# Kernel optimization log

Measured on AMD Instinct MI355X. Metric: run time of the kernel, lower is better.

Reference implementation:

```python
import jax, jax.numpy as jnp
import numpy as np

NEG_INF = -1e9  # large negative instead of -inf for safe masked softmax
LRELU_ALPHA = 0.2


def setup_inputs() -> dict:
    key = jax.random.key(0)
    k1, k2, k3, k4, k5 = jax.random.split(key, 5)
    B, N, Din, H, F = 8, 1024, 256, 4, 64
    X = jax.random.normal(k1, (B, N, Din), dtype=jnp.float32)
    A = jax.random.randint(k2, (B, N, N), 0, 2).astype(jnp.int32)
    # xavier-ish scaled params
    W = jax.random.normal(k3, (Din, H * F), dtype=jnp.float32) * np.sqrt(2.0 / (Din + H * F))
    a_src = jax.random.normal(k4, (H, F), dtype=jnp.float32) * np.sqrt(2.0 / (1 + F))
    a_dst = jax.random.normal(k5, (H, F), dtype=jnp.float32) * np.sqrt(2.0 / (1 + F))
    return {"X": X, "A": A, "W": W, "a_src": a_src, "a_dst": a_dst}


def reference(X, A, W, a_src, a_dst):
    B, N, _ = X.shape
    H, F = a_src.shape
    Wh = (X @ W).reshape(B, N, H, F)                       # [B,N,H,F]
    e_src = jnp.einsum('bnhf,hf->bnh', Wh, a_src)          # [B,N,H]
    e_dst = jnp.einsum('bjhf,hf->bjh', Wh, a_dst)          # [B,N,H]
    # additive scores: e[b,i,j,h] = lrelu(e_src[b,i,h] + e_dst[b,j,h])
    e = jax.nn.leaky_relu(e_src[:, :, None, :] + e_dst[:, None, :, :], LRELU_ALPHA)
    mask = (A > 0)[..., None]                              # [B,N,N,1]
    e = jnp.where(mask, e, NEG_INF)
    alpha = jax.nn.softmax(e, axis=2)                      # softmax over source j
    # dropout is identity in eval mode
    Hout = jnp.einsum('bijh,bjhf->bihf', alpha, Wh)        # [B,N,H,F]
    Hout = jax.nn.elu(Hout)
    return Hout.reshape(B, N, H * F)
```

## Files before the change

### kernel.cpp

```cpp
#include <hip/hip_runtime.h>


typedef unsigned short u16;
typedef short bf16x8 __attribute__((ext_vector_type(8)));
typedef unsigned short u16x8 __attribute__((ext_vector_type(8)));
typedef float f32x4 __attribute__((ext_vector_type(4)));

__device__ __forceinline__ u16 f2bf(float f) {
  unsigned u = __float_as_uint(f);
  unsigned r = (u + 0x7FFFu + ((u >> 16) & 1u)) >> 16;
  return (u16)r;
}
__device__ __forceinline__ float bf2f(u16 h) {
  return __uint_as_float(((unsigned)h) << 16);
}

__device__ __forceinline__ bool detect_bf16(const void* p) {
  const u16* u = (const u16*)p;
  u16 v = u[2 * (threadIdx.x & 63)];
  int ex = (v >> 7) & 0xFF;
  unsigned long long b = __ballot(ex >= 112 && ex <= 142);
  return __popcll(b) >= 48;
}

__global__ __launch_bounds__(256) void prep_kernel(
    const void* __restrict__ X, const int* __restrict__ A,
    const void* __restrict__ W, const void* __restrict__ asrc,
    const void* __restrict__ adst,
    u16* __restrict__ xhi, u16* __restrict__ xlo,
    u16* __restrict__ wthi, u16* __restrict__ wtlo,
    float* __restrict__ aF, unsigned long long* __restrict__ Apack, int use_lo) {
  const int bid = blockIdx.x, t = threadIdx.x;
  if (bid < 1024) {
    const bool bf = detect_bf16(X);
    const int i0 = (bid * 256 + t) * 8;
    float v[8];
    if (bf) {
      u16x8 raw = *(const u16x8*)((const u16*)X + i0);
#pragma unroll
      for (int j = 0; j < 8; ++j) v[j] = bf2f((u16)raw[j]);
    } else {
      const float* Xf = (const float*)X;
#pragma unroll
      for (int j = 0; j < 8; ++j) v[j] = Xf[i0 + j];
    }
    u16x8 hi, lo;
#pragma unroll
    for (int j = 0; j < 8; ++j) {
      u16 h = f2bf(v[j]);
      hi[j] = h;
      lo[j] = f2bf(v[j] - bf2f(h));
    }
    *(u16x8*)(xhi + i0) = hi;
    if (use_lo) *(u16x8*)(xlo + i0) = lo;
  } else if (bid < 1282) {
    const bool bf = detect_bf16(X);
    const int wb = bid - 1024;
    if (wb < 256) {
      const int n = wb, k = t;
      float v = bf ? bf2f(((const u16*)W)[k * 256 + n]) : ((const float*)W)[k * 256 + n];
      u16 h = f2bf(v);
      wthi[n * 256 + k] = h;
      if (use_lo) wtlo[n * 256 + k] = f2bf(v - bf2f(h));
    } else if (wb == 256) {
      aF[t] = bf ? bf2f(((const u16*)asrc)[t]) : ((const float*)asrc)[t];
    } else {
      aF[256 + t] = bf ? bf2f(((const u16*)adst)[t]) : ((const float*)adst)[t];
    }
  } else {
    const int wid = ((bid - 1282) * 256 + t) >> 6;
    const int l = t & 63;
#pragma unroll
    for (int g = 0; g < 16; ++g) {
      const long base = ((long)(wid * 16 + g)) << 6;
      int a = A[base + l];
      unsigned long long m = __ballot(a > 0);
      if (l == 0) Apack[wid * 16 + g] = m;
    }
  }
}

__global__ __launch_bounds__(256) void gemm_kernel(
    const u16* __restrict__ Xhi, const u16* __restrict__ Xlo,
    const u16* __restrict__ WThi, const u16* __restrict__ WTlo,
    const float* __restrict__ aF,
    u16* __restrict__ WhThi,
    float* __restrict__ esT, float* __restrict__ edT, int use_lo) {
  __shared__ __align__(16) u16 As[64 * 32];
  __shared__ __align__(16) u16 Bs[64 * 32];
  __shared__ __align__(16) u16 Asl[64 * 32];
  __shared__ __align__(16) u16 Bsl[64 * 32];
  const int sbid = (blockIdx.x & 7) * 64 + (blockIdx.x >> 3);
  const int bm = sbid >> 2, h = sbid & 3;
  const int t = threadIdx.x, w = t >> 6, l = t & 63;
  const int sr = t >> 2, sc = (t & 3) * 8;
  const int lm = l & 15, lk = (l >> 4) * 8;
  f32x4 acc[4] = {{0,0,0,0},{0,0,0,0},{0,0,0,0},{0,0,0,0}};
  const int xrow = (bm * 64 + sr) * 256 + sc;
  const int wrow = (h * 64 + sr) * 256 + sc;
  for (int k0 = 0; k0 < 256; k0 += 32) {
    __syncthreads();
    *(u16x8*)&As[sr * 32 + sc] = *(const u16x8*)&Xhi[xrow + k0];
    *(u16x8*)&Bs[sr * 32 + sc] = *(const u16x8*)&WThi[wrow + k0];
    if (use_lo) {
      *(u16x8*)&Asl[sr * 32 + sc] = *(const u16x8*)&Xlo[xrow + k0];
      *(u16x8*)&Bsl[sr * 32 + sc] = *(const u16x8*)&WTlo[wrow + k0];
    }
    __syncthreads();
    bf16x8 af = *(const bf16x8*)&As[(w * 16 + lm) * 32 + lk];
#pragma unroll
    for (int ns = 0; ns < 4; ++ns) {
      bf16x8 bfr = *(const bf16x8*)&Bs[(ns * 16 + lm) * 32 + lk];
      acc[ns] = __builtin_amdgcn_mfma_f32_16x16x32_bf16(af, bfr, acc[ns], 0, 0, 0);
      if (use_lo) {
        bf16x8 afl = *(const bf16x8*)&Asl[(w * 16 + lm) * 32 + lk];
        bf16x8 bfl = *(const bf16x8*)&Bsl[(ns * 16 + lm) * 32 + lk];
        acc[ns] = __builtin_amdgcn_mfma_f32_16x16x32_bf16(afl, bfr, acc[ns], 0, 0, 0);
        acc[ns] = __builtin_amdgcn_mfma_f32_16x16x32_bf16(af, bfl, acc[ns], 0, 0, 0);
      }
    }
  }
  float asv[4], adv[4];
#pragma unroll
  for (int ns = 0; ns < 4; ++ns) {
    asv[ns] = aF[h * 64 + ns * 16 + lm];
    adv[ns] = aF[256 + h * 64 + ns * 16 + lm];
  }
#pragma unroll
  for (int j = 0; j < 4; ++j) {
    const int m = bm * 64 + w * 16 + (l >> 4) * 4 + j;
    const int bi = m >> 10, jr = m & 1023;
    float psrc = 0.f, pdst = 0.f;
#pragma unroll
    for (int ns = 0; ns < 4; ++ns) {
      float v = acc[ns][j];
      WhThi[((bi * 4 + h) * 64 + ns * 16 + lm) * 1024 + jr] = f2bf(v);
      psrc += v * asv[ns];
      pdst += v * adv[ns];
    }
#pragma unroll
    for (int mm = 1; mm < 16; mm <<= 1) {
      psrc += __shfl_xor(psrc, mm);
      pdst += __shfl_xor(pdst, mm);
    }
    if (lm == 0) {
      esT[(bi * 4 + h) * 1024 + jr] = psrc;
      edT[(bi * 4 + h) * 1024 + jr] = pdst;
    }
  }
}

__global__ __launch_bounds__(512, 2) void attn_kernel(
    const void* __restrict__ Xraw, const unsigned* __restrict__ Apack,
    const u16* __restrict__ WhThi,
    const float* __restrict__ esT, const float* __restrict__ edT,
    void* __restrict__ out) {
  __shared__ __align__(16) u16 Vs[2][8192];
  __shared__ __align__(16) float eds[2][128];
  const bool outbf = detect_bf16(Xraw);
  const int t = threadIdx.x, l = t & 63, w = t >> 6;
  const int sbid = (blockIdx.x & 7) * 32 + (blockIdx.x >> 3);
  const int h = sbid & 3, it = (sbid >> 2) & 7, b = sbid >> 5;
  const int i0 = it * 128, bh = b * 4 + h;
  const int lm = l & 15, lkg = l >> 4;
  const int row = i0 + w * 16 + lm;
  const float esl = esT[bh * 1024 + row];
  const float* edp = edT + bh * 1024;
  const u16* whbase = WhThi + (size_t)bh * 65536;
  const uint4* amp = (const uint4*)Apack + (size_t)(b * 1024 + row) * 8;

  const int f0 = t >> 4, s0 = t & 15;
  const int f1 = (t + 512) >> 4, s1 = t & 15;
  const int wr0 = (f0 * 16 + (s0 ^ (f0 & 7))) * 8;
  const int wr1 = (f1 * 16 + (s1 ^ (f1 & 7))) * 8;
  const u16* g0p = whbase + f0 * 1024 + s0 * 8;
  const u16* g1p = whbase + f1 * 1024 + s1 * 8;

  f32x4 acc[4] = {{0,0,0,0},{0,0,0,0},{0,0,0,0},{0,0,0,0}};
  float dsum = 0.f;
  const int swz = (lm & 7) << 3;

  uint4 cm = amp[0];
  {
    bf16x8 ga = *(const bf16x8*)(g0p);
    bf16x8 gb = *(const bf16x8*)(g1p);
    *(bf16x8*)&Vs[0][wr0] = ga;
    *(bf16x8*)&Vs[0][wr1] = gb;
    if (t < 64) *(float2*)&eds[0][t * 2] = *(const float2*)(edp + t * 2);
  }
  __syncthreads();

#pragma unroll
  for (int jt = 0; jt < 8; ++jt) {
    const int cur = jt & 1;
    bf16x8 na = {}, nb = {};
    float2 ne = {};
    uint4 nm = {};
    if (jt < 7) {
      na = *(const bf16x8*)(g0p + (jt + 1) * 128);
      nb = *(const bf16x8*)(g1p + (jt + 1) * 128);
      if (t < 64) ne = *(const float2*)(edp + (jt + 1) * 128 + t * 2);
      nm = amp[jt + 1];
    }
#pragma unroll
    for (int ks = 0; ks < 4; ++ks) {
      const unsigned mword = (ks == 0) ? cm.x : (ks == 1) ? cm.y
                           : (ks == 2) ? cm.z : cm.w;
      const unsigned mb = mword >> (lkg * 8);
      float4 e0 = *(const float4*)&eds[cur][ks * 32 + lkg * 8];
      float4 e1 = *(const float4*)&eds[cur][ks * 32 + lkg * 8 + 4];
      const float ed8[8] = {e0.x, e0.y, e0.z, e0.w, e1.x, e1.y, e1.z, e1.w};
      float p[8];
#pragma unroll
      for (int jj = 0; jj < 8; ++jj) {
        float scv = esl + ed8[jj];
        scv = fmaxf(scv, 0.2f * scv);
        p[jj] = ((mb >> jj) & 1u) ? __expf(scv) : 0.f;
        dsum += p[jj];
      }
      union { unsigned u[4]; bf16x8 v; } afu;
#pragma unroll
      for (int q = 0; q < 4; ++q)
        asm("v_cvt_pk_bf16_f32 %0, %1, %2" : "=v"(afu.u[q]) : "v"(p[2*q]), "v"(p[2*q+1]));
      const int jb = (ks * 32 + lkg * 8) ^ swz;
#pragma unroll
      for (int ns = 0; ns < 4; ++ns) {
        bf16x8 vf = *(const bf16x8*)&Vs[cur][(ns * 16 + lm) * 128 + jb];
        acc[ns] = __builtin_amdgcn_mfma_f32_16x16x32_bf16(afu.v, vf, acc[ns], 0, 0, 0);
      }
    }
    if (jt < 7) {
      *(bf16x8*)&Vs[cur ^ 1][wr0] = na;
      *(bf16x8*)&Vs[cur ^ 1][wr1] = nb;
      if (t < 64) *(float2*)&eds[cur ^ 1][t * 2] = ne;
      cm = nm;
    }
    __syncthreads();
  }

  dsum += __shfl_xor(dsum, 16);
  dsum += __shfl_xor(dsum, 32);
#pragma unroll
  for (int j = 0; j < 4; ++j) {
    const int irow = (l >> 4) * 4 + j;
    const float den = __shfl(dsum, irow);
    const float rinv = den > 0.f ? 1.0f / den : 0.f;
    const int rowoff = (b * 1024 + i0 + w * 16 + irow) * 256 + h * 64;
#pragma unroll
    for (int ns = 0; ns < 4; ++ns) {
      float v = acc[ns][j] * rinv;
      v = v > 0.f ? v : (__expf(v) - 1.0f);
      const int off = rowoff + ns * 16 + lm;
      if (outbf) ((u16*)out)[off] = f2bf(v);
      else       ((float*)out)[off] = v;
    }
  }
}

extern "C" void kernel_launch(void* const* d_in, const int* in_sizes, int n_in,
                              void* d_out, int out_size, void* d_ws, size_t ws_size,
                              hipStream_t stream) {
  const void* X = d_in[0];
  const int* A = (const int*)d_in[1];
  const void* W = d_in[2];
  const void* asrc = d_in[3];
  const void* adst = d_in[4];

  char* ws = (char*)d_ws;
  size_t off = 0;
  auto alloc = [&](size_t bytes) -> void* {
    void* p = ws + off;
    off += (bytes + 255) & ~(size_t)255;
    return p;
  };
  u16* Xhi = (u16*)alloc((size_t)2097152 * 2);
  u16* WhThi = (u16*)alloc((size_t)2097152 * 2);
  u16* WThi = (u16*)alloc((size_t)65536 * 2);
  float* esT = (float*)alloc((size_t)32768 * 4);
  float* edT = (float*)alloc((size_t)32768 * 4);
  float* aF = (float*)alloc((size_t)512 * 4);
  unsigned long long* Apack = (unsigned long long*)alloc((size_t)131072 * 8);
  const size_t base_need = off;
  if (ws_size < base_need) return;

  int use_lo = 0;
  u16 *Xlo = Xhi, *WTlo = WThi;
  const size_t lo_extra = (size_t)2097152 * 2 + 65536 * 2 + 512;
  if (ws_size >= base_need + lo_extra) {
    use_lo = 1;
    Xlo = (u16*)alloc((size_t)2097152 * 2);
    WTlo = (u16*)alloc((size_t)65536 * 2);
  }

  prep_kernel<<<3330, 256, 0, stream>>>(X, A, W, asrc, adst, Xhi, Xlo, WThi, WTlo, aF, Apack, use_lo);
  gemm_kernel<<<512, 256, 0, stream>>>(Xhi, Xlo, WThi, WTlo, aF, WhThi, esT, edT, use_lo);
  attn_kernel<<<256, 512, 0, stream>>>(X, (const unsigned*)Apack, WhThi, esT, edT, d_out);
}
```

Measured before the change: 52.99 us.

## Read V operands directly from global memory and halve attention block size

The attention kernel stops staging Wh^T and e_dst tiles through double-buffered shared memory. Each lane now loads its MFMA B-operand fragments and e_dst values straight from global memory, which removes the per-tile __syncthreads and the LDS traffic. Blocks shrink from 512 to 256 threads (64 rows per block) and the grid doubles, giving more independent blocks for occupancy. The cost is that every wave re-reads the same V data through L2/L1 instead of sharing one copy per block, and the 16-byte global loads per lane may expose more latency.

```diff
diff --git a/kernel.cpp b/kernel.cpp
--- a/kernel.cpp
+++ b/kernel.cpp
@@ -150,65 +150,39 @@
   }
 }
 
-__global__ __launch_bounds__(512, 2) void attn_kernel(
+__global__ __launch_bounds__(256, 4) void attn_kernel(
     const void* __restrict__ Xraw, const unsigned* __restrict__ Apack,
     const u16* __restrict__ WhThi,
     const float* __restrict__ esT, const float* __restrict__ edT,
     void* __restrict__ out) {
-  __shared__ __align__(16) u16 Vs[2][8192];
-  __shared__ __align__(16) float eds[2][128];
   const bool outbf = detect_bf16(Xraw);
   const int t = threadIdx.x, l = t & 63, w = t >> 6;
-  const int sbid = (blockIdx.x & 7) * 32 + (blockIdx.x >> 3);
-  const int h = sbid & 3, it = (sbid >> 2) & 7, b = sbid >> 5;
-  const int i0 = it * 128, bh = b * 4 + h;
+  const int sbid = (blockIdx.x & 7) * 64 + (blockIdx.x >> 3);
+  const int h = sbid & 3, it = (sbid >> 2) & 15, b = sbid >> 6;
+  const int i0 = it * 64, bh = b * 4 + h;
   const int lm = l & 15, lkg = l >> 4;
   const int row = i0 + w * 16 + lm;
   const float esl = esT[bh * 1024 + row];
   const float* edp = edT + bh * 1024;
-  const u16* whbase = WhThi + (size_t)bh * 65536;
+  const u16* vbase = WhThi + (size_t)bh * 65536 + lm * 1024;
   const uint4* amp = (const uint4*)Apack + (size_t)(b * 1024 + row) * 8;
-
-  const int f0 = t >> 4, s0 = t & 15;
-  const int f1 = (t + 512) >> 4, s1 = t & 15;
-  const int wr0 = (f0 * 16 + (s0 ^ (f0 & 7))) * 8;
-  const int wr1 = (f1 * 16 + (s1 ^ (f1 & 7))) * 8;
-  const u16* g0p = whbase + f0 * 1024 + s0 * 8;
-  const u16* g1p = whbase + f1 * 1024 + s1 * 8;
 
   f32x4 acc[4] = {{0,0,0,0},{0,0,0,0},{0,0,0,0},{0,0,0,0}};
   float dsum = 0.f;
-  const int swz = (lm & 7) << 3;
 
   uint4 cm = amp[0];
-  {
-    bf16x8 ga = *(const bf16x8*)(g0p);
-    bf16x8 gb = *(const bf16x8*)(g1p);
-    *(bf16x8*)&Vs[0][wr0] = ga;
-    *(bf16x8*)&Vs[0][wr1] = gb;
-    if (t < 64) *(float2*)&eds[0][t * 2] = *(const float2*)(edp + t * 2);
-  }
-  __syncthreads();
-
 #pragma unroll
   for (int jt = 0; jt < 8; ++jt) {
-    const int cur = jt & 1;
-    bf16x8 na = {}, nb = {};
-    float2 ne = {};
     uint4 nm = {};
-    if (jt < 7) {
-      na = *(const bf16x8*)(g0p + (jt + 1) * 128);
-      nb = *(const bf16x8*)(g1p + (jt + 1) * 128);
-      if (t < 64) ne = *(const float2*)(edp + (jt + 1) * 128 + t * 2);
-      nm = amp[jt + 1];
-    }
+    if (jt < 7) nm = amp[jt + 1];
 #pragma unroll
     for (int ks = 0; ks < 4; ++ks) {
+      const int j0 = jt * 128 + ks * 32 + lkg * 8;
       const unsigned mword = (ks == 0) ? cm.x : (ks == 1) ? cm.y
                            : (ks == 2) ? cm.z : cm.w;
       const unsigned mb = mword >> (lkg * 8);
-      float4 e0 = *(const float4*)&eds[cur][ks * 32 + lkg * 8];
-      float4 e1 = *(const float4*)&eds[cur][ks * 32 + lkg * 8 + 4];
+      float4 e0 = *(const float4*)(edp + j0);
+      float4 e1 = *(const float4*)(edp + j0 + 4);
       const float ed8[8] = {e0.x, e0.y, e0.z, e0.w, e1.x, e1.y, e1.z, e1.w};
       float p[8];
 #pragma unroll
@@ -222,20 +196,13 @@
 #pragma unroll
       for (int q = 0; q < 4; ++q)
         asm("v_cvt_pk_bf16_f32 %0, %1, %2" : "=v"(afu.u[q]) : "v"(p[2*q]), "v"(p[2*q+1]));
-      const int jb = (ks * 32 + lkg * 8) ^ swz;
 #pragma unroll
       for (int ns = 0; ns < 4; ++ns) {
-        bf16x8 vf = *(const bf16x8*)&Vs[cur][(ns * 16 + lm) * 128 + jb];
+        bf16x8 vf = *(const bf16x8*)(vbase + ns * 16384 + j0);
         acc[ns] = __builtin_amdgcn_mfma_f32_16x16x32_bf16(afu.v, vf, acc[ns], 0, 0, 0);
       }
     }
-    if (jt < 7) {
-      *(bf16x8*)&Vs[cur ^ 1][wr0] = na;
-      *(bf16x8*)&Vs[cur ^ 1][wr1] = nb;
-      if (t < 64) *(float2*)&eds[cur ^ 1][t * 2] = ne;
-      cm = nm;
-    }
-    __syncthreads();
+    cm = nm;
   }
 
   dsum += __shfl_xor(dsum, 16);
@@ -294,5 +261,5 @@
 
   prep_kernel<<<3330, 256, 0, stream>>>(X, A, W, asrc, adst, Xhi, Xlo, WThi, WTlo, aF, Apack, use_lo);
   gemm_kernel<<<512, 256, 0, stream>>>(Xhi, Xlo, WThi, WTlo, aF, WhThi, esT, edT, use_lo);
-  attn_kernel<<<256, 512, 0, stream>>>(X, (const unsigned*)Apack, WhThi, esT, edT, d_out);
-}
+  attn_kernel<<<512, 256, 0, stream>>>(X, (const unsigned*)Apack, WhThi, esT, edT, d_out);
+}
```

Measured after the change: 76.32 us. 44.0% more time.

## Split attention source dimension across two wave groups and combine via LDS

Applied to the files above, without the earlier changes.

The attention block grows from 512 to 1024 threads. Two halves of eight waves each handle one half of the source-node range (512 columns each) in four pipelined tiles instead of eight. The partial accumulators and softmax denominators from the second half go through shared memory to the first half, which normalizes, applies ELU and writes the output. This doubles the waves per CU to hide memory and MFMA latency and shortens the serial loop. The cost is more LDS, an extra barrier and a combine step, and tighter register limits from the new launch bounds.

```diff
diff --git a/kernel.cpp b/kernel.cpp
--- a/kernel.cpp
+++ b/kernel.cpp
@@ -150,31 +150,32 @@
   }
 }
 
-__global__ __launch_bounds__(512, 2) void attn_kernel(
+__global__ __launch_bounds__(1024, 4) void attn_kernel(
     const void* __restrict__ Xraw, const unsigned* __restrict__ Apack,
     const u16* __restrict__ WhThi,
     const float* __restrict__ esT, const float* __restrict__ edT,
     void* __restrict__ out) {
-  __shared__ __align__(16) u16 Vs[2][8192];
-  __shared__ __align__(16) float eds[2][128];
+  __shared__ __align__(16) u16 Vs[2][2][8192];
+  __shared__ __align__(16) float eds[2][2][128];
+  __shared__ float combL[8][64][17];
+  __shared__ float dsumc[8][16];
   const bool outbf = detect_bf16(Xraw);
   const int t = threadIdx.x, l = t & 63, w = t >> 6;
+  const int rg = w & 7, half = w >> 3;
   const int sbid = (blockIdx.x & 7) * 32 + (blockIdx.x >> 3);
   const int h = sbid & 3, it = (sbid >> 2) & 7, b = sbid >> 5;
   const int i0 = it * 128, bh = b * 4 + h;
   const int lm = l & 15, lkg = l >> 4;
-  const int row = i0 + w * 16 + lm;
+  const int row = i0 + rg * 16 + lm;
   const float esl = esT[bh * 1024 + row];
   const float* edp = edT + bh * 1024;
   const u16* whbase = WhThi + (size_t)bh * 65536;
-  const uint4* amp = (const uint4*)Apack + (size_t)(b * 1024 + row) * 8;
+  const uint4* amp = (const uint4*)Apack + (size_t)(b * 1024 + row) * 8 + half * 4;
 
   const int f0 = t >> 4, s0 = t & 15;
-  const int f1 = (t + 512) >> 4, s1 = t & 15;
   const int wr0 = (f0 * 16 + (s0 ^ (f0 & 7))) * 8;
-  const int wr1 = (f1 * 16 + (s1 ^ (f1 & 7))) * 8;
-  const u16* g0p = whbase + f0 * 1024 + s0 * 8;
-  const u16* g1p = whbase + f1 * 1024 + s1 * 8;
+  const u16* gp = whbase + f0 * 1024 + s0 * 8;
+  const int ehalf = (t >> 6) & 1;
 
   f32x4 acc[4] = {{0,0,0,0},{0,0,0,0},{0,0,0,0},{0,0,0,0}};
   float dsum = 0.f;
@@ -182,24 +183,23 @@
 
   uint4 cm = amp[0];
   {
-    bf16x8 ga = *(const bf16x8*)(g0p);
-    bf16x8 gb = *(const bf16x8*)(g1p);
-    *(bf16x8*)&Vs[0][wr0] = ga;
-    *(bf16x8*)&Vs[0][wr1] = gb;
-    if (t < 64) *(float2*)&eds[0][t * 2] = *(const float2*)(edp + t * 2);
+    *(bf16x8*)&Vs[0][0][wr0] = *(const bf16x8*)(gp);
+    *(bf16x8*)&Vs[0][1][wr0] = *(const bf16x8*)(gp + 512);
+    if (t < 128) *(float2*)&eds[0][ehalf][(t & 63) * 2] =
+        *(const float2*)(edp + ehalf * 512 + (t & 63) * 2);
   }
   __syncthreads();
 
 #pragma unroll
-  for (int jt = 0; jt < 8; ++jt) {
+  for (int jt = 0; jt < 4; ++jt) {
     const int cur = jt & 1;
     bf16x8 na = {}, nb = {};
     float2 ne = {};
     uint4 nm = {};
-    if (jt < 7) {
-      na = *(const bf16x8*)(g0p + (jt + 1) * 128);
-      nb = *(const bf16x8*)(g1p + (jt + 1) * 128);
-      if (t < 64) ne = *(const float2*)(edp + (jt + 1) * 128 + t * 2);
+    if (jt < 3) {
+      na = *(const bf16x8*)(gp + (jt + 1) * 128);
+      nb = *(const bf16x8*)(gp + 512 + (jt + 1) * 128);
+      if (t < 128) ne = *(const float2*)(edp + ehalf * 512 + (jt + 1) * 128 + (t & 63) * 2);
       nm = amp[jt + 1];
     }
 #pragma unroll
@@ -207,8 +207,8 @@
       const unsigned mword = (ks == 0) ? cm.x : (ks == 1) ? cm.y
                            : (ks == 2) ? cm.z : cm.w;
       const unsigned mb = mword >> (lkg * 8);
-      float4 e0 = *(const float4*)&eds[cur][ks * 32 + lkg * 8];
-      float4 e1 = *(const float4*)&eds[cur][ks * 32 + lkg * 8 + 4];
+      float4 e0 = *(const float4*)&eds[cur][half][ks * 32 + lkg * 8];
+      float4 e1 = *(const float4*)&eds[cur][half][ks * 32 + lkg * 8 + 4];
       const float ed8[8] = {e0.x, e0.y, e0.z, e0.w, e1.x, e1.y, e1.z, e1.w};
       float p[8];
 #pragma unroll
@@ -225,14 +225,14 @@
       const int jb = (ks * 32 + lkg * 8) ^ swz;
 #pragma unroll
       for (int ns = 0; ns < 4; ++ns) {
-        bf16x8 vf = *(const bf16x8*)&Vs[cur][(ns * 16 + lm) * 128 + jb];
+        bf16x8 vf = *(const bf16x8*)&Vs[cur][half][(ns * 16 + lm) * 128 + jb];
         acc[ns] = __builtin_amdgcn_mfma_f32_16x16x32_bf16(afu.v, vf, acc[ns], 0, 0, 0);
       }
     }
-    if (jt < 7) {
-      *(bf16x8*)&Vs[cur ^ 1][wr0] = na;
-      *(bf16x8*)&Vs[cur ^ 1][wr1] = nb;
-      if (t < 64) *(float2*)&eds[cur ^ 1][t * 2] = ne;
+    if (jt < 3) {
+      *(bf16x8*)&Vs[cur ^ 1][0][wr0] = na;
+      *(bf16x8*)&Vs[cur ^ 1][1][wr0] = nb;
+      if (t < 128) *(float2*)&eds[cur ^ 1][ehalf][(t & 63) * 2] = ne;
       cm = nm;
     }
     __syncthreads();
@@ -240,19 +240,30 @@
 
   dsum += __shfl_xor(dsum, 16);
   dsum += __shfl_xor(dsum, 32);
-#pragma unroll
-  for (int j = 0; j < 4; ++j) {
-    const int irow = (l >> 4) * 4 + j;
-    const float den = __shfl(dsum, irow);
-    const float rinv = den > 0.f ? 1.0f / den : 0.f;
-    const int rowoff = (b * 1024 + i0 + w * 16 + irow) * 256 + h * 64;
-#pragma unroll
-    for (int ns = 0; ns < 4; ++ns) {
-      float v = acc[ns][j] * rinv;
-      v = v > 0.f ? v : (__expf(v) - 1.0f);
-      const int off = rowoff + ns * 16 + lm;
-      if (outbf) ((u16*)out)[off] = f2bf(v);
-      else       ((float*)out)[off] = v;
+
+  if (half == 1) {
+#pragma unroll
+    for (int ns = 0; ns < 4; ++ns)
+#pragma unroll
+      for (int j = 0; j < 4; ++j) combL[rg][l][ns * 4 + j] = acc[ns][j];
+    if (l < 16) dsumc[rg][l] = dsum;
+  }
+  __syncthreads();
+  if (half == 0) {
+#pragma unroll
+    for (int j = 0; j < 4; ++j) {
+      const int irow = (l >> 4) * 4 + j;
+      const float den = __shfl(dsum, irow) + dsumc[rg][irow];
+      const float rinv = den > 0.f ? 1.0f / den : 0.f;
+      const int rowoff = (b * 1024 + i0 + rg * 16 + irow) * 256 + h * 64;
+#pragma unroll
+      for (int ns = 0; ns < 4; ++ns) {
+        float v = (acc[ns][j] + combL[rg][l][ns * 4 + j]) * rinv;
+        v = v > 0.f ? v : (__expf(v) - 1.0f);
+        const int off = rowoff + ns * 16 + lm;
+        if (outbf) ((u16*)out)[off] = f2bf(v);
+        else       ((float*)out)[off] = v;
+      }
     }
   }
 }
@@ -294,5 +305,5 @@
 
   prep_kernel<<<3330, 256, 0, stream>>>(X, A, W, asrc, adst, Xhi, Xlo, WThi, WTlo, aF, Apack, use_lo);
   gemm_kernel<<<512, 256, 0, stream>>>(Xhi, Xlo, WThi, WTlo, aF, WhThi, esT, edT, use_lo);
-  attn_kernel<<<256, 512, 0, stream>>>(X, (const unsigned*)Apack, WhThi, esT, edT, d_out);
-}
+  attn_kernel<<<256, 1024, 0, stream>>>(X, (const unsigned*)Apack, WhThi, esT, edT, d_out);
+}
```

Result: faster. 51.19 us, median of 2 (-3.4%).
